# Performance work log

Measured on AMD Instinct MI355X. Metric: run time of the kernel, lower is better.

The kernel has to match this reference:

```python
import jax, jax.numpy as jnp
import numpy as np

B, N, F_IN, F_OUT = 4, 4096, 64, 64
ALPHA = 0.2   # leakyrelu negative slope
M_MIX = 0.8   # self.m
NEG_INF = -1e12


def setup_inputs() -> dict:
    key = jax.random.key(0)
    k1, k2, k3, k4 = jax.random.split(key, 4)
    inp = jax.random.normal(k1, (B, N, F_IN), dtype=jnp.float32)
    adj = jax.random.uniform(k2, (B, N, N), dtype=jnp.float32)
    # xavier_uniform with gain=1.414
    limW = 1.414 * np.sqrt(6.0 / (F_IN + F_OUT))
    W = jax.random.uniform(k3, (F_IN, F_OUT), dtype=jnp.float32, minval=-limW, maxval=limW)
    lima = 1.414 * np.sqrt(6.0 / (2 * F_OUT + 1))
    a = jax.random.uniform(k4, (2 * F_OUT, 1), dtype=jnp.float32, minval=-lima, maxval=lima)
    return {"inp": inp, "adj": adj, "W": W, "a": a}


def reference(inp, adj, W, a):
    # h: [B, N, F_OUT]
    h = jnp.einsum("bnf,fo->bno", inp, W)
    # The torch code builds a_input[b,i,j] = [h_i ; h_j], applies leakyrelu
    # elementwise, then contracts with a. Since leakyrelu is elementwise,
    # e[b,i,j] = lrelu(h_i) @ a[:F] + lrelu(h_j) @ a[F:], exactly.
    lh = jax.nn.leaky_relu(h, negative_slope=ALPHA)          # [B, N, F_OUT]
    f_src = lh @ a[:F_OUT, 0]                                # [B, N]  (h_i term)
    f_dst = lh @ a[F_OUT:, 0]                                # [B, N]  (h_j term)
    e = f_src[:, :, None] + f_dst[:, None, :]                # [B, N, N]
    dj = M_MIX * adj + (1.0 - M_MIX) * e
    attention = jnp.where(dj > 0, dj, NEG_INF)
    # torch softmax over dim=1 (the i axis)
    attention = jax.nn.softmax(attention, axis=1)
    # dropout is identity in eval mode
    h_prime = jnp.einsum("bij,bjo->bio", attention, h)       # [B, N, F_OUT]
    return jax.nn.relu(h_prime)
```

## Files before the change

### kernel.cpp

```cpp
#include <hip/hip_runtime.h>
#include <hip/hip_bf16.h>


#define Bn 4
#define Nn 4096
#define KS 8
#define IC 64

typedef _Float16 half8 __attribute__((ext_vector_type(8)));
typedef _Float16 half4 __attribute__((ext_vector_type(4)));
typedef float f32x4 __attribute__((ext_vector_type(4)));
typedef float f4v __attribute__((ext_vector_type(4)));

__global__ __launch_bounds__(256) void k_prep(
    const float* __restrict__ inp, const float* __restrict__ W,
    const float* __restrict__ a, float* __restrict__ h,
    float* __restrict__ fsrc, float* __restrict__ fdst) {
  __shared__ float Ws[64 * 64];
  __shared__ float as[128];
  __shared__ float xs[4][64];
  const int t = threadIdx.x;
  for (int k = t; k < 4096; k += 256) Ws[k] = W[k];
  if (t < 128) as[t] = a[t];
  const int w = t >> 6;
  const int o = t & 63;
  const int row = blockIdx.x * 4 + w;
  xs[w][o] = inp[(size_t)row * 64 + o];
  __syncthreads();
  float acc = 0.f;
  const float* xr = xs[w];
#pragma unroll
  for (int f = 0; f < 64; ++f) acc += xr[f] * Ws[f * 64 + o];
  h[(size_t)row * 64 + o] = acc;
  float lh = acc > 0.f ? acc : 0.2f * acc;
  float vs = lh * as[o];
  float vd = lh * as[64 + o];
#pragma unroll
  for (int off = 32; off > 0; off >>= 1) {
    vs += __shfl_down(vs, off);
    vd += __shfl_down(vd, off);
  }
  if (o == 0) { fsrc[row] = vs; fdst[row] = vd; }
}

__global__ __launch_bounds__(256) void k_estats(
    const float* __restrict__ adj, const float* __restrict__ fsrc,
    const float* __restrict__ fdst, _Float16* __restrict__ E,
    float* __restrict__ pm) {
  const int t = threadIdx.x;
  const int jb = blockIdx.x, ic = blockIdx.y, b = blockIdx.z;
  const int j = jb * 1024 + t * 4;
  const int i0 = ic * 64;
  __shared__ float fss[64];
  if (t < 64) fss[t] = fsrc[b * Nn + i0 + t];
  __syncthreads();
  const float4 fd = *(const float4*)&fdst[b * Nn + j];
  const f4v* ap = (const f4v*)(adj + ((size_t)(b * Nn + i0)) * Nn + j);
  _Float16* ep = E + ((size_t)(b * Nn + i0)) * Nn + j;
  float s0 = 0.f, s1 = 0.f, s2 = 0.f, s3 = 0.f;
#pragma unroll 4
  for (int ii = 0; ii < 64; ++ii) {
    f4v v = __builtin_nontemporal_load(ap + (size_t)ii * 1024);
    float fi = fss[ii];
    float d0 = 0.8f * v.x + 0.2f * (fi + fd.x);
    float d1 = 0.8f * v.y + 0.2f * (fi + fd.y);
    float d2 = 0.8f * v.z + 0.2f * (fi + fd.z);
    float d3 = 0.8f * v.w + 0.2f * (fi + fd.w);
    float e0 = d0 > 0.f ? __expf(d0) : 0.f;
    float e1 = d1 > 0.f ? __expf(d1) : 0.f;
    float e2 = d2 > 0.f ? __expf(d2) : 0.f;
    float e3 = d3 > 0.f ? __expf(d3) : 0.f;
    s0 += e0; s1 += e1; s2 += e2; s3 += e3;
    half4 e;
    e[0] = (_Float16)e0; e[1] = (_Float16)e1;
    e[2] = (_Float16)e2; e[3] = (_Float16)e3;
    *(half4*)(ep + (size_t)ii * Nn) = e;
  }
  float4 sv; sv.x = s0; sv.y = s1; sv.z = s2; sv.w = s3;
  *(float4*)&pm[((size_t)(ic * Bn + b)) * Nn + j] = sv;
}

__global__ __launch_bounds__(256) void k_hscale(
    const float* __restrict__ h, const float* __restrict__ pm,
    _Float16* __restrict__ hT) {
  const int t = threadIdx.x;
  const int jt = blockIdx.x, b = blockIdx.y;
  __shared__ _Float16 hl[64][72];
  __shared__ float sis[64];
  if (t < 64) {
    const int j = jt * 64 + t;
    float sv = 0.f;
#pragma unroll 8
    for (int ic = 0; ic < IC; ++ic) sv += pm[((size_t)(ic * Bn + b)) * Nn + j];
    sis[t] = sv > 0.f ? 1.0f / sv : 0.f;
  }
  __syncthreads();
#pragma unroll
  for (int r = 0; r < 4; ++r) {
    const int jl = r * 16 + (t >> 4);
    const int j = jt * 64 + jl;
    const int o4 = (t & 15) * 4;
    float si = sis[jl];
    float4 hv = *(const float4*)&h[((size_t)(b * Nn + j)) * 64 + o4];
    hl[o4 + 0][jl] = (_Float16)(hv.x * si);
    hl[o4 + 1][jl] = (_Float16)(hv.y * si);
    hl[o4 + 2][jl] = (_Float16)(hv.z * si);
    hl[o4 + 3][jl] = (_Float16)(hv.w * si);
  }
  __syncthreads();
#pragma unroll
  for (int r = 0; r < 2; ++r) {
    const int o = r * 32 + (t >> 3);
    const int ch = t & 7;
    half8 v = *(half8*)&hl[o][ch * 8];
    *(half8*)&hT[((size_t)(b * 64 + o)) * 4096 + jt * 64 + ch * 8] = v;
  }
}

__global__ __launch_bounds__(256) void k_attnmm(
    const _Float16* __restrict__ E, const _Float16* __restrict__ hT,
    float* __restrict__ part) {
  const int t = threadIdx.x;
  const int ks = blockIdx.x;
  const int ib = blockIdx.y;
  const int b = blockIdx.z;
  const int i0 = ib * 64;
  const int kbase = ks * 512;
  const int w = t >> 6;
  const int lane = t & 63;

  __shared__ _Float16 hs[64][136];

  f32x4 acc[4];
#pragma unroll
  for (int nt = 0; nt < 4; ++nt)
#pragma unroll
    for (int r = 0; r < 4; ++r) acc[nt][r] = 0.f;

  const int ai = i0 + w * 16 + (lane & 15);
  const int ko = (lane >> 4) * 8;
  const half8* Erow = (const half8*)(E + ((size_t)(b * Nn + ai)) * Nn + kbase + ko);
  const int so = t >> 2;
  const int sk = (t & 3) * 32;
  const _Float16* hTrow = hT + ((size_t)(b * 64 + so)) * Nn + kbase + sk;

  for (int ch = 0; ch < 4; ++ch) {
    const int k0 = ch * 128;
    __syncthreads();
#pragma unroll
    for (int q = 0; q < 4; ++q) {
      half8 v = *(const half8*)(hTrow + k0 + q * 8);
      *(half8*)&hs[so][sk + q * 8] = v;
    }
    __syncthreads();
#pragma unroll
    for (int kt = 0; kt < 4; ++kt) {
      half8 af = __builtin_nontemporal_load((const half8*)((const _Float16*)Erow + k0 + kt * 32));
#pragma unroll
      for (int nt = 0; nt < 4; ++nt) {
        half8 bf = *(const half8*)&hs[nt * 16 + (lane & 15)][kt * 32 + ko];
        acc[nt] = __builtin_amdgcn_mfma_f32_16x16x32_f16(af, bf, acc[nt], 0, 0, 0);
      }
    }
  }
#pragma unroll
  for (int nt = 0; nt < 4; ++nt)
#pragma unroll
    for (int r = 0; r < 4; ++r) {
      const int i = i0 + w * 16 + (lane >> 4) * 4 + r;
      const int o = nt * 16 + (lane & 15);
      part[(((size_t)ks * Bn + b) * Nn + i) * 64 + o] = acc[nt][r];
    }
}

__global__ __launch_bounds__(256) void k_final(
    const float* __restrict__ part, float* __restrict__ out) {
  const int e = blockIdx.x * 256 + threadIdx.x;
  const f4v* p4 = (const f4v*)part;
  f4v sv = __builtin_nontemporal_load(p4 + e);
  const size_t stride = (size_t)Bn * Nn * 64 / 4;
#pragma unroll
  for (int ks = 1; ks < KS; ++ks) {
    f4v v = __builtin_nontemporal_load(p4 + (size_t)ks * stride + e);
    sv.x += v.x; sv.y += v.y; sv.z += v.z; sv.w += v.w;
  }
  float4 r;
  r.x = fmaxf(sv.x, 0.f); r.y = fmaxf(sv.y, 0.f);
  r.z = fmaxf(sv.z, 0.f); r.w = fmaxf(sv.w, 0.f);
  ((float4*)out)[e] = r;
}

extern "C" void kernel_launch(void* const* d_in, const int* in_sizes, int n_in,
                              void* d_out, int out_size, void* d_ws, size_t ws_size,
                              hipStream_t stream) {
  const float* inp = (const float*)d_in[0];
  const float* adj = (const float*)d_in[1];
  const float* W   = (const float*)d_in[2];
  const float* a   = (const float*)d_in[3];
  float* out = (float*)d_out;

  float* ws   = (float*)d_ws;
  float* h    = ws;
  float* fsrc = h + 1048576;
  float* fdst = fsrc + 16384;
  float* pm   = fdst + 16384;
  float* part = pm + (size_t)IC * Bn * Nn;
  _Float16* hT = (_Float16*)(part + (size_t)KS * Bn * Nn * 64);
  _Float16* E  = hT + (size_t)Bn * 64 * Nn;

  k_prep<<<Bn * Nn / 4, 256, 0, stream>>>(inp, W, a, h, fsrc, fdst);
  k_estats<<<dim3(4, IC, Bn), 256, 0, stream>>>(adj, fsrc, fdst, E, pm);
  k_hscale<<<dim3(64, Bn), 256, 0, stream>>>(h, pm, hT);
  k_attnmm<<<dim3(KS, 64, Bn), 256, 0, stream>>>(E, hT, part);
  k_final<<<Bn * Nn * 64 / 4 / 256, 256, 0, stream>>>(part, out);
}
```

Baseline: 437.7 us.

## Recompute exp attention weights inside matmul instead of materializing fp16 E

Removes the fp16 exponentiated-score matrix E. The column-sum pass now only reads adj and writes per-column partial sums, and the matmul kernel rereads adj, recomputes the masked exp on the fly and feeds it to MFMA. This drops the large write of E and its later read, in exchange for reading fp32 adj twice and doing the exp twice. The split-K factor is halved so each block covers a longer k range, and an occupancy hint is added to the matmul kernel.

```diff
diff --git a/kernel.cpp b/kernel.cpp
--- a/kernel.cpp
+++ b/kernel.cpp
@@ -4,11 +4,10 @@
 
 #define Bn 4
 #define Nn 4096
-#define KS 8
+#define KS 4
 #define IC 64
 
 typedef _Float16 half8 __attribute__((ext_vector_type(8)));
-typedef _Float16 half4 __attribute__((ext_vector_type(4)));
 typedef float f32x4 __attribute__((ext_vector_type(4)));
 typedef float f4v __attribute__((ext_vector_type(4)));
 
@@ -43,10 +42,9 @@
   if (o == 0) { fsrc[row] = vs; fdst[row] = vd; }
 }
 
-__global__ __launch_bounds__(256) void k_estats(
+__global__ __launch_bounds__(256) void k_colsum(
     const float* __restrict__ adj, const float* __restrict__ fsrc,
-    const float* __restrict__ fdst, _Float16* __restrict__ E,
-    float* __restrict__ pm) {
+    const float* __restrict__ fdst, float* __restrict__ pm) {
   const int t = threadIdx.x;
   const int jb = blockIdx.x, ic = blockIdx.y, b = blockIdx.z;
   const int j = jb * 1024 + t * 4;
@@ -55,26 +53,21 @@
   if (t < 64) fss[t] = fsrc[b * Nn + i0 + t];
   __syncthreads();
   const float4 fd = *(const float4*)&fdst[b * Nn + j];
+  const float fd0 = 0.2f * fd.x, fd1 = 0.2f * fd.y, fd2 = 0.2f * fd.z, fd3 = 0.2f * fd.w;
   const f4v* ap = (const f4v*)(adj + ((size_t)(b * Nn + i0)) * Nn + j);
-  _Float16* ep = E + ((size_t)(b * Nn + i0)) * Nn + j;
   float s0 = 0.f, s1 = 0.f, s2 = 0.f, s3 = 0.f;
 #pragma unroll 4
   for (int ii = 0; ii < 64; ++ii) {
-    f4v v = __builtin_nontemporal_load(ap + (size_t)ii * 1024);
-    float fi = fss[ii];
-    float d0 = 0.8f * v.x + 0.2f * (fi + fd.x);
-    float d1 = 0.8f * v.y + 0.2f * (fi + fd.y);
-    float d2 = 0.8f * v.z + 0.2f * (fi + fd.z);
-    float d3 = 0.8f * v.w + 0.2f * (fi + fd.w);
-    float e0 = d0 > 0.f ? __expf(d0) : 0.f;
-    float e1 = d1 > 0.f ? __expf(d1) : 0.f;
-    float e2 = d2 > 0.f ? __expf(d2) : 0.f;
-    float e3 = d3 > 0.f ? __expf(d3) : 0.f;
-    s0 += e0; s1 += e1; s2 += e2; s3 += e3;
-    half4 e;
-    e[0] = (_Float16)e0; e[1] = (_Float16)e1;
-    e[2] = (_Float16)e2; e[3] = (_Float16)e3;
-    *(half4*)(ep + (size_t)ii * Nn) = e;
+    f4v v = ap[(size_t)ii * 1024];
+    float fi = 0.2f * fss[ii];
+    float d0 = 0.8f * v.x + (fi + fd0);
+    float d1 = 0.8f * v.y + (fi + fd1);
+    float d2 = 0.8f * v.z + (fi + fd2);
+    float d3 = 0.8f * v.w + (fi + fd3);
+    s0 += d0 > 0.f ? __expf(d0) : 0.f;
+    s1 += d1 > 0.f ? __expf(d1) : 0.f;
+    s2 += d2 > 0.f ? __expf(d2) : 0.f;
+    s3 += d3 > 0.f ? __expf(d3) : 0.f;
   }
   float4 sv; sv.x = s0; sv.y = s1; sv.z = s2; sv.w = s3;
   *(float4*)&pm[((size_t)(ic * Bn + b)) * Nn + j] = sv;
@@ -117,17 +110,20 @@
   }
 }
 
-__global__ __launch_bounds__(256) void k_attnmm(
-    const _Float16* __restrict__ E, const _Float16* __restrict__ hT,
+__global__ __launch_bounds__(256, 4) void k_attnmm(
+    const float* __restrict__ adj, const _Float16* __restrict__ hT,
+    const float* __restrict__ fsrc, const float* __restrict__ fdst,
     float* __restrict__ part) {
   const int t = threadIdx.x;
   const int ks = blockIdx.x;
   const int ib = blockIdx.y;
   const int b = blockIdx.z;
   const int i0 = ib * 64;
-  const int kbase = ks * 512;
+  const int kbase = ks * 1024;
   const int w = t >> 6;
   const int lane = t & 63;
+  const int m = lane & 15;
+  const int q = lane >> 4;
 
   __shared__ _Float16 hs[64][136];
 
@@ -137,28 +133,51 @@
 #pragma unroll
     for (int r = 0; r < 4; ++r) acc[nt][r] = 0.f;
 
-  const int ai = i0 + w * 16 + (lane & 15);
-  const int ko = (lane >> 4) * 8;
-  const half8* Erow = (const half8*)(E + ((size_t)(b * Nn + ai)) * Nn + kbase + ko);
+  const int ai = i0 + w * 16 + m;
+  const float fs2 = 0.2f * fsrc[b * Nn + ai];
+  const float* arow = adj + ((size_t)(b * Nn + ai)) * Nn + kbase;
+  const float* fdr = fdst + b * Nn + kbase;
+
   const int so = t >> 2;
   const int sk = (t & 3) * 32;
   const _Float16* hTrow = hT + ((size_t)(b * 64 + so)) * Nn + kbase + sk;
 
-  for (int ch = 0; ch < 4; ++ch) {
+  for (int ch = 0; ch < 8; ++ch) {
     const int k0 = ch * 128;
     __syncthreads();
 #pragma unroll
-    for (int q = 0; q < 4; ++q) {
-      half8 v = *(const half8*)(hTrow + k0 + q * 8);
-      *(half8*)&hs[so][sk + q * 8] = v;
+    for (int qq = 0; qq < 4; ++qq) {
+      half8 v = *(const half8*)(hTrow + k0 + qq * 8);
+      *(half8*)&hs[so][sk + qq * 8] = v;
     }
     __syncthreads();
 #pragma unroll
     for (int kt = 0; kt < 4; ++kt) {
-      half8 af = __builtin_nontemporal_load((const half8*)((const _Float16*)Erow + k0 + kt * 32));
+      const int kc = k0 + kt * 32 + q * 8;
+      f4v v0 = __builtin_nontemporal_load((const f4v*)(arow + kc));
+      f4v v1 = __builtin_nontemporal_load((const f4v*)(arow + kc + 4));
+      float4 fdA = *(const float4*)(fdr + kc);
+      float4 fdB = *(const float4*)(fdr + kc + 4);
+      float d0 = 0.8f * v0.x + (fs2 + 0.2f * fdA.x);
+      float d1 = 0.8f * v0.y + (fs2 + 0.2f * fdA.y);
+      float d2 = 0.8f * v0.z + (fs2 + 0.2f * fdA.z);
+      float d3 = 0.8f * v0.w + (fs2 + 0.2f * fdA.w);
+      float d4 = 0.8f * v1.x + (fs2 + 0.2f * fdB.x);
+      float d5 = 0.8f * v1.y + (fs2 + 0.2f * fdB.y);
+      float d6 = 0.8f * v1.z + (fs2 + 0.2f * fdB.z);
+      float d7 = 0.8f * v1.w + (fs2 + 0.2f * fdB.w);
+      half8 af;
+      af[0] = (_Float16)(d0 > 0.f ? __expf(d0) : 0.f);
+      af[1] = (_Float16)(d1 > 0.f ? __expf(d1) : 0.f);
+      af[2] = (_Float16)(d2 > 0.f ? __expf(d2) : 0.f);
+      af[3] = (_Float16)(d3 > 0.f ? __expf(d3) : 0.f);
+      af[4] = (_Float16)(d4 > 0.f ? __expf(d4) : 0.f);
+      af[5] = (_Float16)(d5 > 0.f ? __expf(d5) : 0.f);
+      af[6] = (_Float16)(d6 > 0.f ? __expf(d6) : 0.f);
+      af[7] = (_Float16)(d7 > 0.f ? __expf(d7) : 0.f);
 #pragma unroll
       for (int nt = 0; nt < 4; ++nt) {
-        half8 bf = *(const half8*)&hs[nt * 16 + (lane & 15)][kt * 32 + ko];
+        half8 bf = *(const half8*)&hs[nt * 16 + m][kt * 32 + q * 8];
         acc[nt] = __builtin_amdgcn_mfma_f32_16x16x32_f16(af, bf, acc[nt], 0, 0, 0);
       }
     }
@@ -167,8 +186,8 @@
   for (int nt = 0; nt < 4; ++nt)
 #pragma unroll
     for (int r = 0; r < 4; ++r) {
-      const int i = i0 + w * 16 + (lane >> 4) * 4 + r;
-      const int o = nt * 16 + (lane & 15);
+      const int i = i0 + w * 16 + q * 4 + r;
+      const int o = nt * 16 + m;
       part[(((size_t)ks * Bn + b) * Nn + i) * 64 + o] = acc[nt][r];
     }
 }
@@ -206,11 +225,10 @@
   float* pm   = fdst + 16384;
   float* part = pm + (size_t)IC * Bn * Nn;
   _Float16* hT = (_Float16*)(part + (size_t)KS * Bn * Nn * 64);
-  _Float16* E  = hT + (size_t)Bn * 64 * Nn;
 
   k_prep<<<Bn * Nn / 4, 256, 0, stream>>>(inp, W, a, h, fsrc, fdst);
-  k_estats<<<dim3(4, IC, Bn), 256, 0, stream>>>(adj, fsrc, fdst, E, pm);
+  k_colsum<<<dim3(4, IC, Bn), 256, 0, stream>>>(adj, fsrc, fdst, pm);
   k_hscale<<<dim3(64, Bn), 256, 0, stream>>>(h, pm, hT);
-  k_attnmm<<<dim3(KS, 64, Bn), 256, 0, stream>>>(E, hT, part);
+  k_attnmm<<<dim3(KS, 64, Bn), 256, 0, stream>>>(adj, hT, fsrc, fdst, part);
   k_final<<<Bn * Nn * 64 / 4 / 256, 256, 0, stream>>>(part, out);
 }
```

New measurement: 449.2 us. 2.6% more time.
